# Kernel tuning notes

Measured on AMD Instinct MI355X. Metric: run time of the kernel, lower is better.

## Reference

```python
import jax, jax.numpy as jnp
import numpy as np

ALPHA = 2.8
R_ONSET = 1.7
R_CUTOFF = 2.0
N, C, BOX = 4096, 16, 40.0


def setup_inputs() -> dict:
    key = jax.random.key(0)
    k1, k2, k3, k4 = jax.random.split(key, 4)
    position = jax.random.uniform(k1, (N, 3), dtype=jnp.float32) * BOX
    celltype = jax.random.uniform(k2, (N, C), dtype=jnp.float32)
    epsilon = jax.random.normal(k3, (N, C * C), dtype=jnp.float32)
    radius = jax.random.uniform(k4, (N, 1), dtype=jnp.float32) * 0.5 + 0.5
    return {"position": position, "celltype": celltype, "epsilon": epsilon, "radius": radius}


def _smooth_cutoff(dr):
    # jax_md multiplicative isotropic cutoff (smooth switch r_onset -> r_cutoff, in r^2)
    r = dr * dr
    r_o = R_ONSET ** 2
    r_c = R_CUTOFF ** 2
    inner = jnp.where(dr < R_CUTOFF,
                      (r_c - r) ** 2 * (r_c + 2.0 * r - 3.0 * r_o) / (r_c - r_o) ** 3,
                      0.0)
    return jnp.where(dr < R_ONSET, 1.0, inner)


def reference(position, celltype, epsilon, radius):
    n, c = celltype.shape
    # --- per-particle epsilon matrices, symmetrized ---
    # 0.5*(triu+tril.T+triu.T+tril) minus diag-correction == 0.5*(M+M.T) with diag M_ii
    E = epsilon.reshape(n, c, c)  # (N,C,C)
    E_sym = 0.5 * (E + jnp.swapaxes(E, 1, 2))  # diagonal already equals M_ii
    # --- bilinear celltype dot products ---
    # A[i,j] = ct_i^T E_sym_i ct_j ; eps[i,j] = 0.5*(A[i,j]+A[j,i])
    A = jnp.einsum('ic,icd,jd->ij', celltype, E_sym, celltype)  # (N,N)
    eps_mat = 0.5 * (A + A.T)
    eps_mat = 5.0 * jax.nn.sigmoid(eps_mat) + 0.3
    # mask columns where celltype sums to zero (broadcast over rows)
    eps_mat = jnp.where(celltype.sum(-1) > 0.0, eps_mat, 0.0)
    # --- sigma matrix ---
    sigma = radius + radius.T  # (N,N)
    # --- pairwise distances (free space displacement) ---
    d = position[:, None, :] - position[None, :, :]  # (N,N,3)
    r2 = jnp.sum(d * d, axis=-1)
    dr = jnp.sqrt(jnp.where(r2 > 0.0, r2, 1.0))  # safe sqrt for diagonal
    # --- morse pair energy with multiplicative cutoff ---
    u = 1.0 - jnp.exp(-ALPHA * (dr - sigma))
    e = (eps_mat * u * u - eps_mat) * _smooth_cutoff(dr)
    mask = 1.0 - jnp.eye(n, dtype=e.dtype)
    return 0.5 * jnp.sum(mask * e)
```

## Files before the change

### kernel.cpp

```cpp
#include <hip/hip_runtime.h>

#define NPART 4096
#define CT    16
#define ALPHA 2.8f
#define R_ON   1.7f
#define R_C2   4.0f
#define INV_DEN (1.0f / 1.367631f)
#define TJ 64

__global__ __launch_bounds__(256) void prep_kernel(
        const float* __restrict__ pos,
        const float* __restrict__ ct,
        const float* __restrict__ eps,
        const float* __restrict__ rad,
        float* __restrict__ w,
        float* __restrict__ maskv,
        float4* __restrict__ posr,
        float* __restrict__ out) {
    int t = blockIdx.x * blockDim.x + threadIdx.x;
    int i = t >> 4;
    int d = t & 15;
    const float* Ei  = eps + i * (CT * CT);
    const float* cti = ct + i * CT;
    float acc = 0.f;
#pragma unroll
    for (int c = 0; c < CT; ++c)
        acc += cti[c] * 0.5f * (Ei[c * CT + d] + Ei[d * CT + c]);
    w[i * CT + d] = acc;
    if (d == 0) {
        float s = 0.f;
#pragma unroll
        for (int c = 0; c < CT; ++c) s += cti[c];
        maskv[i] = (s > 0.f) ? 1.f : 0.f;
        posr[i] = make_float4(pos[3 * i], pos[3 * i + 1], pos[3 * i + 2], rad[i]);
    }
    if (t == 0) *out = 0.f;
}

__global__ __launch_bounds__(256) void pair_kernel(
        const float4* __restrict__ posr,
        const float* __restrict__ ct,
        const float* __restrict__ w,
        const float* __restrict__ maskv,
        float* __restrict__ out) {
    __shared__ float4 tile[TJ];
    __shared__ float wsum_s[4];
    const int tid = threadIdx.x;
    const int i   = blockIdx.x * 256 + tid;
    const int j0  = blockIdx.y * TJ;

    if (tid < TJ) tile[tid] = posr[j0 + tid];
    const float4 pi = posr[i];
    __syncthreads();

    unsigned long long hits = 0ull;
#pragma unroll 8
    for (int jj = 0; jj < TJ; ++jj) {
        float4 pj = tile[jj];
        float dx = pi.x - pj.x, dy = pi.y - pj.y, dz = pi.z - pj.z;
        float r2 = dx * dx + dy * dy + dz * dz;
        if ((j0 + jj) != i && r2 < R_C2) hits |= (1ull << jj);
    }

    float acc = 0.f;
    if (hits) {
        float cti[CT], wi[CT];
        const float4* ct4 = (const float4*)(ct + i * CT);
        const float4* w4  = (const float4*)(w + i * CT);
#pragma unroll
        for (int q = 0; q < 4; ++q) {
            float4 v = ct4[q];
            cti[4 * q] = v.x; cti[4 * q + 1] = v.y; cti[4 * q + 2] = v.z; cti[4 * q + 3] = v.w;
            float4 u = w4[q];
            wi[4 * q] = u.x; wi[4 * q + 1] = u.y; wi[4 * q + 2] = u.z; wi[4 * q + 3] = u.w;
        }
        while (hits) {
            int jj = __builtin_ctzll(hits);
            hits &= hits - 1;
            int j = j0 + jj;
            float4 pj = tile[jj];
            float dx = pi.x - pj.x, dy = pi.y - pj.y, dz = pi.z - pj.z;
            float r2 = dx * dx + dy * dy + dz * dz;
            float dr = sqrtf(r2 > 0.f ? r2 : 1.f);
            float cut;
            if (dr < R_ON) {
                cut = 1.f;
            } else {
                float t1 = R_C2 - r2;
                cut = t1 * t1 * (2.f * r2 - 4.67f) * INV_DEN;
            }
            const float4* ctj4 = (const float4*)(ct + j * CT);
            const float4* wj4  = (const float4*)(w + j * CT);
            float a = 0.f, b = 0.f;
#pragma unroll
            for (int q = 0; q < 4; ++q) {
                float4 cv = ctj4[q];
                float4 wv = wj4[q];
                a += wi[4 * q] * cv.x + wi[4 * q + 1] * cv.y + wi[4 * q + 2] * cv.z + wi[4 * q + 3] * cv.w;
                b += cti[4 * q] * wv.x + cti[4 * q + 1] * wv.y + cti[4 * q + 2] * wv.z + cti[4 * q + 3] * wv.w;
            }
            float bb   = 0.5f * (a + b);
            float epsv = maskv[j] * (5.f / (1.f + __expf(-bb)) + 0.3f);
            float sigma = pi.w + pj.w;
            float u = 1.f - __expf(-ALPHA * (dr - sigma));
            acc += epsv * (u * u - 1.f) * cut;
        }
    }

#pragma unroll
    for (int off = 32; off; off >>= 1) acc += __shfl_down(acc, off, 64);
    int lane = tid & 63, wv = tid >> 6;
    if (lane == 0) wsum_s[wv] = acc;
    __syncthreads();
    if (tid == 0) atomicAdd(out, 0.5f * (wsum_s[0] + wsum_s[1] + wsum_s[2] + wsum_s[3]));
}

extern "C" void kernel_launch(void* const* d_in, const int* in_sizes, int n_in,
                              void* d_out, int out_size, void* d_ws, size_t ws_size,
                              hipStream_t stream) {
    const float* pos = (const float*)d_in[0];
    const float* ct  = (const float*)d_in[1];
    const float* eps = (const float*)d_in[2];
    const float* rad = (const float*)d_in[3];
    float* out = (float*)d_out;

    char* ws = (char*)d_ws;
    float*  w     = (float*)ws;
    float4* posr  = (float4*)(ws + 256 * 1024);
    float*  maskv = (float*)(ws + 320 * 1024);

    prep_kernel<<<NPART * CT / 256, 256, 0, stream>>>(pos, ct, eps, rad, w, maskv, posr, out);
    dim3 grid(NPART / 256, NPART / TJ);
    pair_kernel<<<grid, 256, 0, stream>>>(posr, ct, w, maskv, out);
}
```

Baseline: 81.06 us.

## Stage epsilon in LDS for prep and drop hit-mask pass in pair kernel

The prep kernel now loads each block's 16 epsilon matrices and celltype rows into shared memory with coalesced float4 loads, then reads the transposed entries from LDS instead of making strided global reads. The pair kernel drops the LDS position tile and the two-pass bitmask of hits, and instead loops over j, reading positions straight from global memory and evaluating the pair only when it falls inside the cutoff. It also preloads the i-row celltype and weights unconditionally, and swaps the sigmoid division for a hardware reciprocal. This trades the bitmask bookkeeping and a barrier for more divergent inline branching and uncached-broadcast global loads, and the j-side dot products now use scalar loads rather than float4.

```diff
diff --git a/kernel.cpp b/kernel.cpp
--- a/kernel.cpp
+++ b/kernel.cpp
@@ -6,7 +6,8 @@
 #define R_ON   1.7f
 #define R_C2   4.0f
 #define INV_DEN (1.0f / 1.367631f)
-#define TJ 64
+#define JC 64
+#define PPB 16
 
 __global__ __launch_bounds__(256) void prep_kernel(
         const float* __restrict__ pos,
@@ -17,24 +18,42 @@
         float* __restrict__ maskv,
         float4* __restrict__ posr,
         float* __restrict__ out) {
-    int t = blockIdx.x * blockDim.x + threadIdx.x;
-    int i = t >> 4;
-    int d = t & 15;
-    const float* Ei  = eps + i * (CT * CT);
-    const float* cti = ct + i * CT;
+    __shared__ float S[PPB][260];
+    __shared__ float CTs[PPB][16];
+    const int tid = threadIdx.x;
+    const int p0  = blockIdx.x * PPB;
+
+    const float4* e4 = (const float4*)(eps + p0 * (CT * CT));
+#pragma unroll
+    for (int q = tid; q < PPB * 64; q += 256) {
+        float4 v = e4[q];
+        int pp = q >> 6;
+        int fo = (q & 63) << 2;
+        *(float4*)&S[pp][fo] = v;
+    }
+    if (tid < 64) {
+        int row = tid >> 2, qq = (tid & 3) << 2;
+        *(float4*)&CTs[row][qq] = *(const float4*)(ct + (p0 + row) * CT + qq);
+    }
+    __syncthreads();
+
+    const int p = tid >> 4;
+    const int d = tid & 15;
     float acc = 0.f;
 #pragma unroll
     for (int c = 0; c < CT; ++c)
-        acc += cti[c] * 0.5f * (Ei[c * CT + d] + Ei[d * CT + c]);
+        acc += CTs[p][c] * 0.5f * (S[p][c * CT + d] + S[p][d * CT + c]);
+    const int i = p0 + p;
     w[i * CT + d] = acc;
+
     if (d == 0) {
         float s = 0.f;
 #pragma unroll
-        for (int c = 0; c < CT; ++c) s += cti[c];
+        for (int c = 0; c < CT; ++c) s += CTs[p][c];
         maskv[i] = (s > 0.f) ? 1.f : 0.f;
         posr[i] = make_float4(pos[3 * i], pos[3 * i + 1], pos[3 * i + 2], rad[i]);
     }
-    if (t == 0) *out = 0.f;
+    if (tid == 0 && blockIdx.x == 0) *out = 0.f;
 }
 
 __global__ __launch_bounds__(256) void pair_kernel(
@@ -43,45 +62,31 @@
         const float* __restrict__ w,
         const float* __restrict__ maskv,
         float* __restrict__ out) {
-    __shared__ float4 tile[TJ];
     __shared__ float wsum_s[4];
     const int tid = threadIdx.x;
     const int i   = blockIdx.x * 256 + tid;
-    const int j0  = blockIdx.y * TJ;
+    const int j0  = blockIdx.y * JC;
 
-    if (tid < TJ) tile[tid] = posr[j0 + tid];
     const float4 pi = posr[i];
-    __syncthreads();
-
-    unsigned long long hits = 0ull;
-#pragma unroll 8
-    for (int jj = 0; jj < TJ; ++jj) {
-        float4 pj = tile[jj];
-        float dx = pi.x - pj.x, dy = pi.y - pj.y, dz = pi.z - pj.z;
-        float r2 = dx * dx + dy * dy + dz * dz;
-        if ((j0 + jj) != i && r2 < R_C2) hits |= (1ull << jj);
+    float cti[CT], wi[CT];
+    const float4* ct4 = (const float4*)(ct + i * CT);
+    const float4* w4  = (const float4*)(w + i * CT);
+#pragma unroll
+    for (int q = 0; q < 4; ++q) {
+        float4 v = ct4[q];
+        cti[4 * q] = v.x; cti[4 * q + 1] = v.y; cti[4 * q + 2] = v.z; cti[4 * q + 3] = v.w;
+        float4 u = w4[q];
+        wi[4 * q] = u.x; wi[4 * q + 1] = u.y; wi[4 * q + 2] = u.z; wi[4 * q + 3] = u.w;
     }
 
     float acc = 0.f;
-    if (hits) {
-        float cti[CT], wi[CT];
-        const float4* ct4 = (const float4*)(ct + i * CT);
-        const float4* w4  = (const float4*)(w + i * CT);
-#pragma unroll
-        for (int q = 0; q < 4; ++q) {
-            float4 v = ct4[q];
-            cti[4 * q] = v.x; cti[4 * q + 1] = v.y; cti[4 * q + 2] = v.z; cti[4 * q + 3] = v.w;
-            float4 u = w4[q];
-            wi[4 * q] = u.x; wi[4 * q + 1] = u.y; wi[4 * q + 2] = u.z; wi[4 * q + 3] = u.w;
-        }
-        while (hits) {
-            int jj = __builtin_ctzll(hits);
-            hits &= hits - 1;
-            int j = j0 + jj;
-            float4 pj = tile[jj];
-            float dx = pi.x - pj.x, dy = pi.y - pj.y, dz = pi.z - pj.z;
-            float r2 = dx * dx + dy * dy + dz * dz;
-            float dr = sqrtf(r2 > 0.f ? r2 : 1.f);
+#pragma unroll 4
+    for (int j = j0; j < j0 + JC; ++j) {
+        float4 pj = posr[j];
+        float dx = pi.x - pj.x, dy = pi.y - pj.y, dz = pi.z - pj.z;
+        float r2 = dx * dx + dy * dy + dz * dz;
+        if (r2 < R_C2 && j != i) {
+            float dr = sqrtf(r2);
             float cut;
             if (dr < R_ON) {
                 cut = 1.f;
@@ -89,18 +94,16 @@
                 float t1 = R_C2 - r2;
                 cut = t1 * t1 * (2.f * r2 - 4.67f) * INV_DEN;
             }
-            const float4* ctj4 = (const float4*)(ct + j * CT);
-            const float4* wj4  = (const float4*)(w + j * CT);
+            const float* ctj = ct + j * CT;
+            const float* wj  = w + j * CT;
             float a = 0.f, b = 0.f;
 #pragma unroll
-            for (int q = 0; q < 4; ++q) {
-                float4 cv = ctj4[q];
-                float4 wv = wj4[q];
-                a += wi[4 * q] * cv.x + wi[4 * q + 1] * cv.y + wi[4 * q + 2] * cv.z + wi[4 * q + 3] * cv.w;
-                b += cti[4 * q] * wv.x + cti[4 * q + 1] * wv.y + cti[4 * q + 2] * wv.z + cti[4 * q + 3] * wv.w;
+            for (int c = 0; c < CT; ++c) {
+                a += wi[c] * ctj[c];
+                b += cti[c] * wj[c];
             }
             float bb   = 0.5f * (a + b);
-            float epsv = maskv[j] * (5.f / (1.f + __expf(-bb)) + 0.3f);
+            float epsv = maskv[j] * (5.f * __builtin_amdgcn_rcpf(1.f + __expf(-bb)) + 0.3f);
             float sigma = pi.w + pj.w;
             float u = 1.f - __expf(-ALPHA * (dr - sigma));
             acc += epsv * (u * u - 1.f) * cut;
@@ -129,7 +132,7 @@
     float4* posr  = (float4*)(ws + 256 * 1024);
     float*  maskv = (float*)(ws + 320 * 1024);
 
-    prep_kernel<<<NPART * CT / 256, 256, 0, stream>>>(pos, ct, eps, rad, w, maskv, posr, out);
-    dim3 grid(NPART / 256, NPART / TJ);
+    prep_kernel<<<NPART / PPB, 256, 0, stream>>>(pos, ct, eps, rad, w, maskv, posr, out);
+    dim3 grid(NPART / 256, NPART / JC);
     pair_kernel<<<grid, 256, 0, stream>>>(posr, ct, w, maskv, out);
 }
```

Result: slower. 85.40 us (+5.4%).
